# Performance work log

Hardware: AMD Instinct MI355X
Metric: run time of the kernel (lower is better)

## Reference

```python
import jax, jax.numpy as jnp
import numpy as np

N_NODES = 100000


def setup_inputs() -> dict:
    key = jax.random.key(0)
    ks = jax.random.split(key, 7)
    N, F, C, K, E = N_NODES, 64, 32, 3, 1_600_000
    x = jax.random.normal(ks[0], (N, F), dtype=jnp.float32)
    edge_vals = jax.random.uniform(ks[1], (K, E), dtype=jnp.float32)
    W = jax.random.normal(ks[2], (F, C), dtype=jnp.float32) / np.sqrt(F)
    b = jax.random.normal(ks[3], (C,), dtype=jnp.float32) * 0.01
    alpha = jnp.ones((K,), dtype=jnp.float32)
    edge_rows = jax.random.randint(ks[4], (K, E), 0, N, dtype=jnp.int64 if jax.config.jax_enable_x64 else jnp.int32)
    edge_cols = jax.random.randint(ks[5], (K, E), 0, N, dtype=jnp.int64 if jax.config.jax_enable_x64 else jnp.int32)
    return {"x": x, "edge_vals": edge_vals, "W": W, "b": b, "alpha": alpha,
            "edge_rows": edge_rows, "edge_cols": edge_cols}


def reference(x, edge_vals, W, b, alpha, edge_rows, edge_cols):
    # Fused form of: (sum_k alpha[k] * A_k) @ x, then Linear.
    # Per hop k: agg_k[n] = sum_{e: rows[k,e]==n} vals[k,e] * x[cols[k,e]]
    def hop_spmm(vals, rows, cols):
        msg = vals[:, None] * x[cols]                      # [E, F] gather + scale
        return jax.ops.segment_sum(msg, rows, num_segments=N_NODES)  # [N, F]

    agg = jax.vmap(hop_spmm)(edge_vals, edge_rows, edge_cols)  # [K, N, F]
    h = jnp.einsum('k,knf->nf', alpha, agg)                    # weighted hop sum
    return h @ W + b                                           # [N, C]
```

## Files before the change

### kernel.cpp

```cpp
#include <hip/hip_runtime.h>

#define N_NODES 100000
#define F 64
#define C 32
#define KH 3
#define E 1600000
#define NE (KH * E)

#define NSLICE 4
#define SLICEW 25000
#define NKEY (N_NODES * NSLICE)
#define KPB 512
#define NBUCK ((NKEY + KPB - 1) / KPB)
#define HCHUNK 4096
#define NHCHUNK ((NE + HCHUNK - 1) / HCHUNK)
#define CHUNK1 8192
#define NCHUNK1 ((NE + CHUNK1 - 1) / CHUNK1)
#define P2CAP 8192
#define GEMM_BLOCKS ((N_NODES * 2 + 255) / 256)

__global__ __launch_bounds__(256) void gemm_hist_k(const float* __restrict__ x,
                                                   const float* __restrict__ W,
                                                   float* __restrict__ y,
                                                   const int* __restrict__ rows,
                                                   int* __restrict__ hcnt) {
    __shared__ float smem[F * C];

    if (blockIdx.x < GEMM_BLOCKS) {
        float* Ws = smem;
        for (int i = threadIdx.x; i < F * C; i += 256) Ws[i] = W[i];
        __syncthreads();

        const int g = blockIdx.x * 256 + threadIdx.x;
        if (g >= N_NODES * 2) return;
        const int node = g >> 1;
        const int h = (g & 1) * 16;

        const float4* xp = (const float4*)(x + (size_t)node * F);
        float acc[16];
#pragma unroll
        for (int c = 0; c < 16; c++) acc[c] = 0.f;

#pragma unroll
        for (int i = 0; i < 16; i++) {
            float4 v = xp[i];
            const int f = i * 4;
#pragma unroll
            for (int c = 0; c < 16; c++) {
                acc[c] += v.x * Ws[(f + 0) * C + h + c];
                acc[c] += v.y * Ws[(f + 1) * C + h + c];
                acc[c] += v.z * Ws[(f + 2) * C + h + c];
                acc[c] += v.w * Ws[(f + 3) * C + h + c];
            }
        }

        float4* yo = (float4*)(y + (size_t)node * C + h);
#pragma unroll
        for (int i = 0; i < 4; i++)
            yo[i] = make_float4(acc[4 * i], acc[4 * i + 1], acc[4 * i + 2], acc[4 * i + 3]);
    } else {
        int* hh = (int*)smem;
        for (int i = threadIdx.x; i < NBUCK; i += 256) hh[i] = 0;
        __syncthreads();
        const int base = (blockIdx.x - GEMM_BLOCKS) * HCHUNK;
#pragma unroll
        for (int j = 0; j < 4; j++) {
            const int e = base + j * 1024 + threadIdx.x * 4;
            if (e + 3 < NE) {
                const int4 r4 = *(const int4*)(rows + e);
                atomicAdd(&hh[r4.x >> 7], 1);
                atomicAdd(&hh[r4.y >> 7], 1);
                atomicAdd(&hh[r4.z >> 7], 1);
                atomicAdd(&hh[r4.w >> 7], 1);
            }
        }
        __syncthreads();
        for (int i = threadIdx.x; i < NBUCK; i += 256) {
            const int cc = hh[i];
            if (cc) atomicAdd(&hcnt[i], cc);
        }
    }
}

__global__ __launch_bounds__(256) void scan_c(const int* __restrict__ hcnt,
                                              int* __restrict__ bstart,
                                              int* __restrict__ bcur,
                                              int* __restrict__ rs_start) {
    __shared__ int sA[1024], sB[1024];
    const int tid = threadIdx.x;
    for (int i = tid; i < 1024; i += 256) sA[i] = (i < NBUCK) ? hcnt[i] : 0;
    __syncthreads();
    int* src = sA;
    int* dst = sB;
    for (int d = 1; d < 1024; d <<= 1) {
        for (int i = tid; i < 1024; i += 256) {
            int v = src[i];
            if (i >= d) v += src[i - d];
            dst[i] = v;
        }
        __syncthreads();
        int* t = src; src = dst; dst = t;
    }
    for (int i = tid; i < NBUCK; i += 256) {
        const int excl = (i == 0) ? 0 : src[i - 1];
        bstart[i] = excl;
        bcur[i] = excl;
    }
    if (tid == 0) {
        bstart[NBUCK] = NE;
        rs_start[NKEY] = NE;
    }
}

__global__ __launch_bounds__(512) void part1_k(const float* __restrict__ vals,
                                               const int* __restrict__ rows,
                                               const int* __restrict__ cols,
                                               const float* __restrict__ alpha,
                                               int* __restrict__ bcur,
                                               int2* __restrict__ edgebuf) {
    __shared__ int sA[1024];
    __shared__ int wtot[8];
    __shared__ int lpos[NBUCK];
    __shared__ int lbase[NBUCK];
    __shared__ int2 stage[CHUNK1];
    __shared__ unsigned short sbin[CHUNK1];

    const int tid = threadIdx.x;
    const int base = blockIdx.x * CHUNK1;

    for (int i = tid; i < 1024; i += 512) sA[i] = 0;
    __syncthreads();

    int kj[16], cj[16];
    float wj[16];
#pragma unroll
    for (int j = 0; j < 4; j++) {
        const int e = base + j * 2048 + tid * 4;
        if (e + 3 < NE) {
            const int4   r4 = *(const int4*)(rows + e);
            const int4   c4 = *(const int4*)(cols + e);
            const float4 v4 = *(const float4*)(vals + e);
            const float ak = alpha[(e >= 2 * E) ? 2 : (e >= E) ? 1 : 0];
            kj[j * 4 + 0] = r4.x * NSLICE + c4.x / SLICEW; cj[j * 4 + 0] = c4.x; wj[j * 4 + 0] = v4.x * ak;
            kj[j * 4 + 1] = r4.y * NSLICE + c4.y / SLICEW; cj[j * 4 + 1] = c4.y; wj[j * 4 + 1] = v4.y * ak;
            kj[j * 4 + 2] = r4.z * NSLICE + c4.z / SLICEW; cj[j * 4 + 2] = c4.z; wj[j * 4 + 2] = v4.z * ak;
            kj[j * 4 + 3] = r4.w * NSLICE + c4.w / SLICEW; cj[j * 4 + 3] = c4.w; wj[j * 4 + 3] = v4.w * ak;
            atomicAdd(&sA[kj[j * 4 + 0] >> 9], 1);
            atomicAdd(&sA[kj[j * 4 + 1] >> 9], 1);
            atomicAdd(&sA[kj[j * 4 + 2] >> 9], 1);
            atomicAdd(&sA[kj[j * 4 + 3] >> 9], 1);
        } else {
            kj[j * 4 + 0] = kj[j * 4 + 1] = kj[j * 4 + 2] = kj[j * 4 + 3] = -1;
        }
    }
    __syncthreads();

    {
        const int lane = tid & 63;
        const int w = tid >> 6;
        const int b2 = tid * 2;
        const int a0 = sA[b2], a1 = sA[b2 + 1];
        const int l1 = a0 + a1;
        int sc = l1;
#pragma unroll
        for (int d = 1; d < 64; d <<= 1) {
            int u = __shfl_up(sc, d);
            if (lane >= d) sc += u;
        }
        if (lane == 63) wtot[w] = sc;
        __syncthreads();
        int wb = 0;
#pragma unroll
        for (int q = 0; q < 8; q++)
            if (q < w) wb += wtot[q];
        const int tb = wb + sc - l1;
        sA[b2] = tb + a0; sA[b2 + 1] = tb + l1;
    }
    __syncthreads();

    for (int i = tid; i < NBUCK; i += 512) {
        const int excl = (i == 0) ? 0 : sA[i - 1];
        const int cnt = sA[i] - excl;
        lpos[i] = excl;
        if (cnt) lbase[i] = atomicAdd(&bcur[i], cnt);
    }
    __syncthreads();

#pragma unroll
    for (int j = 0; j < 16; j++) {
        if (kj[j] >= 0) {
            const int b = kj[j] >> 9;
            const int p = atomicAdd(&lpos[b], 1);
            stage[p] = make_int2(((kj[j] & (KPB - 1)) << 17) | cj[j],
                                 __float_as_int(wj[j]));
            sbin[p] = (unsigned short)b;
        }
    }
    __syncthreads();

    const int total = sA[1023];
    for (int p = tid; p < total; p += 512) {
        const int b = sbin[p];
        const int excl = (b == 0) ? 0 : sA[b - 1];
        edgebuf[lbase[b] + (p - excl)] = stage[p];
    }
}

__global__ __launch_bounds__(512) void part2_k(const int* __restrict__ bstart,
                                               int* __restrict__ rs_start,
                                               int2* __restrict__ edgebuf) {
    __shared__ int2 sstage[P2CAP];
    __shared__ int sh[KPB];
    __shared__ int sg[KPB];
    __shared__ int wtot[8];
    __shared__ int lbin[KPB];

    const int tid = threadIdx.x;
    const int b = blockIdx.x;
    const int bs = bstart[b];
    const int be = bstart[b + 1];
    const int n = be - bs;

    for (int k = tid; k < KPB; k += 512) sh[k] = 0;
    __syncthreads();

    if (n <= P2CAP) {
        for (int i = tid; i < n; i += 512) {
            const int2 e = edgebuf[bs + i];
            sstage[i] = e;
            atomicAdd(&sh[((unsigned)e.x) >> 17], 1);
        }
    }
    __syncthreads();

    {
        const int lane = tid & 63;
        const int w = tid >> 6;
        const int a0 = sh[tid];
        int sc = a0;
#pragma unroll
        for (int d = 1; d < 64; d <<= 1) {
            int u = __shfl_up(sc, d);
            if (lane >= d) sc += u;
        }
        if (lane == 63) wtot[w] = sc;
        __syncthreads();
        int wb = 0;
#pragma unroll
        for (int q = 0; q < 8; q++)
            if (q < w) wb += wtot[q];
        sg[tid] = wb + sc;
    }
    __syncthreads();

    for (int k = tid; k < KPB; k += 512) {
        const int st = bs + ((k == 0) ? 0 : sg[k - 1]);
        lbin[k] = st;
        const int idx = (b << 9) + k;
        if (idx < NKEY) rs_start[idx] = st;
    }
    __syncthreads();

    if (n > P2CAP) return;

    for (int i = tid; i < n; i += 512) {
        const int2 e = sstage[i];
        const int sub = ((unsigned)e.x) >> 17;
        const int pos = atomicAdd(&lbin[sub], 1);
        edgebuf[pos] = e;
    }
}

__global__ __launch_bounds__(256) void gathers9_k(const long long* __restrict__ eb,
                                                  const int* __restrict__ rs_start,
                                                  const float* __restrict__ y,
                                                  const float* __restrict__ bias,
                                                  float* __restrict__ out) {
    const int blk = blockIdx.x;
    const int s = blk & (NSLICE - 1);
    const int row = (blk >> 2) * 8 + (threadIdx.x >> 5);
    const int c = threadIdx.x & 31;
    const int key = row * NSLICE + s;
    const int st = rs_start[key];
    const int en = rs_start[key + 1];

    float acc = (s == 0) ? bias[c] : 0.f;

    int i = st;
    for (; i + 8 <= en; i += 8) {
        const long long l0 = __builtin_nontemporal_load(&eb[i + 0]);
        const long long l1 = __builtin_nontemporal_load(&eb[i + 1]);
        const long long l2 = __builtin_nontemporal_load(&eb[i + 2]);
        const long long l3 = __builtin_nontemporal_load(&eb[i + 3]);
        const long long l4 = __builtin_nontemporal_load(&eb[i + 4]);
        const long long l5 = __builtin_nontemporal_load(&eb[i + 5]);
        const long long l6 = __builtin_nontemporal_load(&eb[i + 6]);
        const long long l7 = __builtin_nontemporal_load(&eb[i + 7]);
        const float y0 = y[(((int)l0) & 0x1FFFF) * C + c];
        const float y1 = y[(((int)l1) & 0x1FFFF) * C + c];
        const float y2 = y[(((int)l2) & 0x1FFFF) * C + c];
        const float y3 = y[(((int)l3) & 0x1FFFF) * C + c];
        const float y4 = y[(((int)l4) & 0x1FFFF) * C + c];
        const float y5 = y[(((int)l5) & 0x1FFFF) * C + c];
        const float y6 = y[(((int)l6) & 0x1FFFF) * C + c];
        const float y7 = y[(((int)l7) & 0x1FFFF) * C + c];
        acc += __int_as_float((int)(l0 >> 32)) * y0;
        acc += __int_as_float((int)(l1 >> 32)) * y1;
        acc += __int_as_float((int)(l2 >> 32)) * y2;
        acc += __int_as_float((int)(l3 >> 32)) * y3;
        acc += __int_as_float((int)(l4 >> 32)) * y4;
        acc += __int_as_float((int)(l5 >> 32)) * y5;
        acc += __int_as_float((int)(l6 >> 32)) * y6;
        acc += __int_as_float((int)(l7 >> 32)) * y7;
    }
    for (; i + 4 <= en; i += 4) {
        const long long l0 = __builtin_nontemporal_load(&eb[i + 0]);
        const long long l1 = __builtin_nontemporal_load(&eb[i + 1]);
        const long long l2 = __builtin_nontemporal_load(&eb[i + 2]);
        const long long l3 = __builtin_nontemporal_load(&eb[i + 3]);
        const float y0 = y[(((int)l0) & 0x1FFFF) * C + c];
        const float y1 = y[(((int)l1) & 0x1FFFF) * C + c];
        const float y2 = y[(((int)l2) & 0x1FFFF) * C + c];
        const float y3 = y[(((int)l3) & 0x1FFFF) * C + c];
        acc += __int_as_float((int)(l0 >> 32)) * y0;
        acc += __int_as_float((int)(l1 >> 32)) * y1;
        acc += __int_as_float((int)(l2 >> 32)) * y2;
        acc += __int_as_float((int)(l3 >> 32)) * y3;
    }
    for (; i < en; i++) {
        const long long l0 = __builtin_nontemporal_load(&eb[i]);
        acc += __int_as_float((int)(l0 >> 32)) * y[(((int)l0) & 0x1FFFF) * C + c];
    }

    unsafeAtomicAdd(out + (size_t)row * C + c, acc);
}

__global__ __launch_bounds__(256) void scatter_edges(
    const float* __restrict__ vals, const int* __restrict__ rows,
    const int* __restrict__ cols, const float* __restrict__ alpha,
    const float* __restrict__ y, float* __restrict__ out_acc) {
    const int t = blockIdx.x * 256 + threadIdx.x;
    const int e = t >> 5;
    const int c = t & 31;
    if (e >= KH * E) return;
    const int k = (e >= 2 * E) ? 2 : (e >= E) ? 1 : 0;
    const float w = vals[e] * alpha[k];
    const float yv = y[(size_t)cols[e] * C + c];
    unsafeAtomicAdd(out_acc + (size_t)rows[e] * C + c, w * yv);
}

__global__ __launch_bounds__(256) void gemm_only_k(const float* __restrict__ x,
                                                   const float* __restrict__ W,
                                                   float* __restrict__ y) {
    __shared__ float Ws[F * C];
    for (int i = threadIdx.x; i < F * C; i += 256) Ws[i] = W[i];
    __syncthreads();
    const int g = blockIdx.x * 256 + threadIdx.x;
    if (g >= N_NODES * 2) return;
    const int node = g >> 1;
    const int h = (g & 1) * 16;
    const float4* xp = (const float4*)(x + (size_t)node * F);
    float acc[16];
#pragma unroll
    for (int c = 0; c < 16; c++) acc[c] = 0.f;
#pragma unroll
    for (int i = 0; i < 16; i++) {
        float4 v = xp[i];
        const int f = i * 4;
#pragma unroll
        for (int c = 0; c < 16; c++) {
            acc[c] += v.x * Ws[(f + 0) * C + h + c];
            acc[c] += v.y * Ws[(f + 1) * C + h + c];
            acc[c] += v.z * Ws[(f + 2) * C + h + c];
            acc[c] += v.w * Ws[(f + 3) * C + h + c];
        }
    }
    float4* yo = (float4*)(y + (size_t)node * C + h);
#pragma unroll
    for (int i = 0; i < 4; i++)
        yo[i] = make_float4(acc[4 * i], acc[4 * i + 1], acc[4 * i + 2], acc[4 * i + 3]);
}

__global__ __launch_bounds__(256) void finalize_k(float* __restrict__ out,
                                                  const float* __restrict__ bias) {
    const int idx = (blockIdx.x * 256 + threadIdx.x) * 4;
    if (idx >= N_NODES * C) return;
    const int c0 = idx & (C - 1);
    float4 v = *(float4*)(out + idx);
    v.x += bias[c0 + 0];
    v.y += bias[c0 + 1];
    v.z += bias[c0 + 2];
    v.w += bias[c0 + 3];
    *(float4*)(out + idx) = v;
}

extern "C" void kernel_launch(void* const* d_in, const int* in_sizes, int n_in,
                              void* d_out, int out_size, void* d_ws, size_t ws_size,
                              hipStream_t stream) {
    const float* x         = (const float*)d_in[0];
    const float* edge_vals = (const float*)d_in[1];
    const float* W         = (const float*)d_in[2];
    const float* b         = (const float*)d_in[3];
    const float* alpha     = (const float*)d_in[4];
    const int*   edge_rows = (const int*)d_in[5];
    const int*   edge_cols = (const int*)d_in[6];
    float*       out       = (float*)d_out;

    const size_t offY   = 0;
    const size_t offEB  = (size_t)N_NODES * C * 4;
    const size_t offRS  = offEB + (size_t)NE * 8;
    const size_t offBS  = offRS + (((size_t)(NKEY + 1) * 4 + 255) & ~(size_t)255);
    const size_t offBC  = offBS + (((NBUCK + 1) * 4 + 255) & ~(size_t)255);
    const size_t offHC  = offBC + ((NBUCK * 4 + 255) & ~(size_t)255);
    const size_t need   = offHC + (size_t)NBUCK * 4;

    float* y = (float*)((char*)d_ws + offY);

    if (ws_size >= need) {
        int2* edgebuf  = (int2*)((char*)d_ws + offEB);
        int*  rs_start = (int*)((char*)d_ws + offRS);
        int*  bstart   = (int*)((char*)d_ws + offBS);
        int*  bcur     = (int*)((char*)d_ws + offBC);
        int*  hcnt     = (int*)((char*)d_ws + offHC);

        hipMemsetAsync(hcnt, 0, (size_t)NBUCK * 4, stream);
        hipMemsetAsync(out, 0, (size_t)N_NODES * C * sizeof(float), stream);

        gemm_hist_k<<<GEMM_BLOCKS + NHCHUNK, 256, 0, stream>>>(
            x, W, y, edge_rows, hcnt);
        scan_c<<<1, 256, 0, stream>>>(hcnt, bstart, bcur, rs_start);
        part1_k<<<NCHUNK1, 512, 0, stream>>>(edge_vals, edge_rows, edge_cols,
                                             alpha, bcur, edgebuf);
        part2_k<<<NBUCK, 512, 0, stream>>>(bstart, rs_start, edgebuf);
        gathers9_k<<<(N_NODES / 8) * NSLICE, 256, 0, stream>>>(
            (const long long*)edgebuf, rs_start, y, b, out);
    } else {
        gemm_only_k<<<GEMM_BLOCKS, 256, 0, stream>>>(x, W, y);
        hipMemsetAsync(out, 0, (size_t)N_NODES * C * sizeof(float), stream);
        const long long scatter_threads = (long long)KH * E * C;
        const int scatter_blocks = (int)((scatter_threads + 255) / 256);
        scatter_edges<<<scatter_blocks, 256, 0, stream>>>(
            edge_vals, edge_rows, edge_cols, alpha, y, out);
        finalize_k<<<(N_NODES * C / 4 + 255) / 256, 256, 0, stream>>>(out, b);
    }
}
```

Before: 355.4 us.

## Widen part1 blocks, stage part2 scatter in LDS, split gather atomics into partials

New measurement: 349.1 us. Within noise of the previous version (-1.8%).

```diff
diff --git a/kernel.cpp b/kernel.cpp
--- a/kernel.cpp
+++ b/kernel.cpp
@@ -112,14 +112,14 @@
     }
 }
 
-__global__ __launch_bounds__(512) void part1_k(const float* __restrict__ vals,
-                                               const int* __restrict__ rows,
-                                               const int* __restrict__ cols,
-                                               const float* __restrict__ alpha,
-                                               int* __restrict__ bcur,
-                                               int2* __restrict__ edgebuf) {
+__global__ __launch_bounds__(1024) void part1_k(const float* __restrict__ vals,
+                                                const int* __restrict__ rows,
+                                                const int* __restrict__ cols,
+                                                const float* __restrict__ alpha,
+                                                int* __restrict__ bcur,
+                                                int2* __restrict__ edgebuf) {
     __shared__ int sA[1024];
-    __shared__ int wtot[8];
+    __shared__ int wtot[16];
     __shared__ int lpos[NBUCK];
     __shared__ int lbase[NBUCK];
     __shared__ int2 stage[CHUNK1];
@@ -128,14 +128,14 @@
     const int tid = threadIdx.x;
     const int base = blockIdx.x * CHUNK1;
 
-    for (int i = tid; i < 1024; i += 512) sA[i] = 0;
-    __syncthreads();
-
-    int kj[16], cj[16];
-    float wj[16];
-#pragma unroll
-    for (int j = 0; j < 4; j++) {
-        const int e = base + j * 2048 + tid * 4;
+    sA[tid] = 0;
+    __syncthreads();
+
+    int kj[8], cj[8];
+    float wj[8];
+#pragma unroll
+    for (int j = 0; j < 2; j++) {
+        const int e = base + j * 4096 + tid * 4;
         if (e + 3 < NE) {
             const int4   r4 = *(const int4*)(rows + e);
             const int4   c4 = *(const int4*)(cols + e);
@@ -158,10 +158,8 @@
     {
         const int lane = tid & 63;
         const int w = tid >> 6;
-        const int b2 = tid * 2;
-        const int a0 = sA[b2], a1 = sA[b2 + 1];
-        const int l1 = a0 + a1;
-        int sc = l1;
+        const int a0 = sA[tid];
+        int sc = a0;
 #pragma unroll
         for (int d = 1; d < 64; d <<= 1) {
             int u = __shfl_up(sc, d);
@@ -171,23 +169,22 @@
         __syncthreads();
         int wb = 0;
 #pragma unroll
-        for (int q = 0; q < 8; q++)
+        for (int q = 0; q < 16; q++)
             if (q < w) wb += wtot[q];
-        const int tb = wb + sc - l1;
-        sA[b2] = tb + a0; sA[b2 + 1] = tb + l1;
-    }
-    __syncthreads();
-
-    for (int i = tid; i < NBUCK; i += 512) {
-        const int excl = (i == 0) ? 0 : sA[i - 1];
-        const int cnt = sA[i] - excl;
-        lpos[i] = excl;
-        if (cnt) lbase[i] = atomicAdd(&bcur[i], cnt);
-    }
-    __syncthreads();
-
-#pragma unroll
-    for (int j = 0; j < 16; j++) {
+        sA[tid] = wb + sc;
+    }
+    __syncthreads();
+
+    if (tid < NBUCK) {
+        const int excl = (tid == 0) ? 0 : sA[tid - 1];
+        const int cnt = sA[tid] - excl;
+        lpos[tid] = excl;
+        if (cnt) lbase[tid] = atomicAdd(&bcur[tid], cnt);
+    }
+    __syncthreads();
+
+#pragma unroll
+    for (int j = 0; j < 8; j++) {
         if (kj[j] >= 0) {
             const int b = kj[j] >> 9;
             const int p = atomicAdd(&lpos[b], 1);
@@ -199,7 +196,7 @@
     __syncthreads();
 
     const int total = sA[1023];
-    for (int p = tid; p < total; p += 512) {
+    for (int p = tid; p < total; p += 1024) {
         const int b = sbin[p];
         const int excl = (b == 0) ? 0 : sA[b - 1];
         edgebuf[lbase[b] + (p - excl)] = stage[p];
@@ -227,7 +224,6 @@
     if (n <= P2CAP) {
         for (int i = tid; i < n; i += 512) {
             const int2 e = edgebuf[bs + i];
-            sstage[i] = e;
             atomicAdd(&sh[((unsigned)e.x) >> 17], 1);
         }
     }
@@ -254,28 +250,35 @@
     __syncthreads();
 
     for (int k = tid; k < KPB; k += 512) {
-        const int st = bs + ((k == 0) ? 0 : sg[k - 1]);
-        lbin[k] = st;
+        const int rel = (k == 0) ? 0 : sg[k - 1];
+        lbin[k] = rel;
         const int idx = (b << 9) + k;
-        if (idx < NKEY) rs_start[idx] = st;
+        if (idx < NKEY) rs_start[idx] = bs + rel;
     }
     __syncthreads();
 
     if (n > P2CAP) return;
 
     for (int i = tid; i < n; i += 512) {
-        const int2 e = sstage[i];
+        const int2 e = edgebuf[bs + i];
         const int sub = ((unsigned)e.x) >> 17;
         const int pos = atomicAdd(&lbin[sub], 1);
-        edgebuf[pos] = e;
-    }
-}
-
-__global__ __launch_bounds__(256) void gathers9_k(const long long* __restrict__ eb,
-                                                  const int* __restrict__ rs_start,
-                                                  const float* __restrict__ y,
-                                                  const float* __restrict__ bias,
-                                                  float* __restrict__ out) {
+        sstage[pos] = e;
+    }
+    __syncthreads();
+
+    for (int i = tid; i < n; i += 512) {
+        edgebuf[bs + i] = sstage[i];
+    }
+}
+
+__global__ __launch_bounds__(256) void gathers9p_k(const long long* __restrict__ eb,
+                                                   const int* __restrict__ rs_start,
+                                                   const float* __restrict__ y,
+                                                   const float* __restrict__ bias,
+                                                   float* __restrict__ out,
+                                                   float* __restrict__ parts,
+                                                   const int mode) {
     const int blk = blockIdx.x;
     const int s = blk & (NSLICE - 1);
     const int row = (blk >> 2) * 8 + (threadIdx.x >> 5);
@@ -332,7 +335,23 @@
         acc += __int_as_float((int)(l0 >> 32)) * y[(((int)l0) & 0x1FFFF) * C + c];
     }
 
-    unsafeAtomicAdd(out + (size_t)row * C + c, acc);
+    if (mode) {
+        unsafeAtomicAdd(out + (size_t)row * C + c, acc);
+    } else if (s == 0) {
+        __builtin_nontemporal_store(acc, out + (size_t)row * C + c);
+    } else {
+        unsafeAtomicAdd(parts + (size_t)row * C + c, acc);
+    }
+}
+
+__global__ __launch_bounds__(256) void reduce2_k(float* __restrict__ out,
+                                                 const float* __restrict__ parts) {
+    const int idx = (blockIdx.x * 256 + threadIdx.x) * 4;
+    if (idx >= N_NODES * C) return;
+    float4 v = *(float4*)(out + idx);
+    const float4 a = *(const float4*)(parts + idx);
+    v.x += a.x; v.y += a.y; v.z += a.z; v.w += a.w;
+    *(float4*)(out + idx) = v;
 }
 
 __global__ __launch_bounds__(256) void scatter_edges(
@@ -412,28 +431,37 @@
     const size_t offBS  = offRS + (((size_t)(NKEY + 1) * 4 + 255) & ~(size_t)255);
     const size_t offBC  = offBS + (((NBUCK + 1) * 4 + 255) & ~(size_t)255);
     const size_t offHC  = offBC + ((NBUCK * 4 + 255) & ~(size_t)255);
-    const size_t need   = offHC + (size_t)NBUCK * 4;
+    const size_t offP   = (offHC + (size_t)NBUCK * 4 + 255) & ~(size_t)255;
+    const size_t need_mid   = offP;
+    const size_t need_parts = offP + (size_t)N_NODES * C * 4;
 
     float* y = (float*)((char*)d_ws + offY);
 
-    if (ws_size >= need) {
+    if (ws_size >= need_mid) {
         int2* edgebuf  = (int2*)((char*)d_ws + offEB);
         int*  rs_start = (int*)((char*)d_ws + offRS);
         int*  bstart   = (int*)((char*)d_ws + offBS);
         int*  bcur     = (int*)((char*)d_ws + offBC);
         int*  hcnt     = (int*)((char*)d_ws + offHC);
+        float* parts   = (float*)((char*)d_ws + offP);
+        const int mode = (ws_size >= need_parts) ? 0 : 1;
 
         hipMemsetAsync(hcnt, 0, (size_t)NBUCK * 4, stream);
-        hipMemsetAsync(out, 0, (size_t)N_NODES * C * sizeof(float), stream);
+        if (mode == 0)
+            hipMemsetAsync(parts, 0, (size_t)N_NODES * C * sizeof(float), stream);
+        else
+            hipMemsetAsync(out, 0, (size_t)N_NODES * C * sizeof(float), stream);
 
         gemm_hist_k<<<GEMM_BLOCKS + NHCHUNK, 256, 0, stream>>>(
             x, W, y, edge_rows, hcnt);
         scan_c<<<1, 256, 0, stream>>>(hcnt, bstart, bcur, rs_start);
-        part1_k<<<NCHUNK1, 512, 0, stream>>>(edge_vals, edge_rows, edge_cols,
-                                             alpha, bcur, edgebuf);
+        part1_k<<<NCHUNK1, 1024, 0, stream>>>(edge_vals, edge_rows, edge_cols,
+                                              alpha, bcur, edgebuf);
         part2_k<<<NBUCK, 512, 0, stream>>>(bstart, rs_start, edgebuf);
-        gathers9_k<<<(N_NODES / 8) * NSLICE, 256, 0, stream>>>(
-            (const long long*)edgebuf, rs_start, y, b, out);
+        gathers9p_k<<<(N_NODES / 8) * NSLICE, 256, 0, stream>>>(
+            (const long long*)edgebuf, rs_start, y, b, out, parts, mode);
+        if (mode == 0)
+            reduce2_k<<<(N_NODES * C / 4 + 255) / 256, 256, 0, stream>>>(out, parts);
     } else {
         gemm_only_k<<<GEMM_BLOCKS, 256, 0, stream>>>(x, W, y);
         hipMemsetAsync(out, 0, (size_t)N_NODES * C * sizeof(float), stream);
```
